# Optimization experiments

Measured on AMD Instinct MI355X. Metric: run time of the kernel, lower is better.

The kernel has to match this reference:

```python
import jax, jax.numpy as jnp
import numpy as np

S, B, D, H, L = 1024, 2, 1024, 16, 4
HD = D // H            # 64
MLP = 4 * D            # 4096
EPS = 1e-5


def _ln(x, w, b):
    m = x.mean(-1, keepdims=True)
    v = ((x - m) ** 2).mean(-1, keepdims=True)
    return (x - m) * jax.lax.rsqrt(v + EPS) * w + b


def _rotate_half(x):
    h = x.shape[-1] // 2
    return jnp.concatenate([-x[..., h:], x[..., :h]], axis=-1)


def _rope(t, cos, sin):
    # t: (B, S, H, HD); cos/sin: (S, HD) broadcast to (1, S, 1, HD)
    return t * cos[None, :, None, :] + _rotate_half(t) * sin[None, :, None, :]


def setup_inputs() -> dict:
    key = jax.random.key(0)
    ks = iter(jax.random.split(key, 64))

    def p(shape, scale=0.02):
        return jax.random.normal(next(ks), shape, jnp.float32) * scale

    return {
        "x": jax.random.normal(next(ks), (S, B, D), jnp.float32),
        "rotary_pos_emb": jax.random.normal(next(ks), (S, HD // 2), jnp.float32),
        # stacked per-layer params (leading dim L) for lax.scan
        "ln1_w": jnp.ones((L, D), jnp.float32), "ln1_b": jnp.zeros((L, D), jnp.float32),
        "in_w": p((L, 3 * D, D)), "in_b": jnp.zeros((L, 3 * D), jnp.float32),
        "out_w": p((L, D, D)), "out_b": jnp.zeros((L, D), jnp.float32),
        "ln2_w": jnp.ones((L, D), jnp.float32), "ln2_b": jnp.zeros((L, D), jnp.float32),
        "fc_w": p((L, MLP, D)), "fc_b": jnp.zeros((L, MLP), jnp.float32),
        "cp_w": p((L, D, MLP)), "cp_b": jnp.zeros((L, D), jnp.float32),
        # attention pooling head (qkv_bias=False in CrossAttention)
        "pn_q_w": jnp.ones((D,), jnp.float32), "pn_q_b": jnp.zeros((D,), jnp.float32),
        "pn_k_w": jnp.ones((D,), jnp.float32), "pn_k_b": jnp.zeros((D,), jnp.float32),
        "pn_v_w": jnp.ones((D,), jnp.float32), "pn_v_b": jnp.zeros((D,), jnp.float32),
        "pq_w": p((D, D)), "pk_w": p((D, D)), "pv_w": p((D, D)),
        "pp_w": p((D, D)), "pp_b": jnp.zeros((D,), jnp.float32),
    }


def reference(x, rotary_pos_emb, ln1_w, ln1_b, in_w, in_b, out_w, out_b,
              ln2_w, ln2_b, fc_w, fc_b, cp_w, cp_b,
              pn_q_w, pn_q_b, pn_k_w, pn_k_b, pn_v_w, pn_v_b,
              pq_w, pk_w, pv_w, pp_w, pp_b):
    # freqs (S, HD/2) -> cos/sin tiled twice along last dim: (S, HD)
    cos = jnp.tile(jnp.cos(rotary_pos_emb), (1, 2))
    sin = jnp.tile(jnp.sin(rotary_pos_emb), (1, 2))
    scale = 1.0 / np.sqrt(HD).astype(np.float32)

    def layer(h, p):
        l1w, l1b, iw, ib, ow, ob, l2w, l2b, fw, fb, cw, cb = p
        a = _ln(h, l1w, l1b)
        qkv = jnp.einsum('sbd,ed->sbe', a, iw) + ib           # (S,B,3D)
        qkv = qkv.reshape(S, B, 3, H, HD)
        q = jnp.transpose(qkv[:, :, 0], (1, 0, 2, 3))          # (B,S,H,HD)
        k = jnp.transpose(qkv[:, :, 1], (1, 0, 2, 3))
        v = jnp.transpose(qkv[:, :, 2], (1, 0, 2, 3))
        q = _rope(q, cos, sin)
        k = _rope(k, cos, sin)
        q, k, v = (t.transpose(0, 2, 1, 3) for t in (q, k, v))  # (B,H,S,HD)
        attn = jax.nn.softmax(jnp.einsum('bhsd,bhtd->bhst', q, k) * scale, axis=-1)
        o = jnp.einsum('bhst,bhtd->bhsd', attn, v)
        o = o.transpose(2, 0, 1, 3).reshape(S, B, D)           # back to (S,B,D)
        h = h + jnp.einsum('sbd,ed->sbe', o, ow) + ob          # residual + out_proj
        m = _ln(h, l2w, l2b)
        m = jax.nn.gelu(jnp.einsum('sbd,ed->sbe', m, fw) + fb, approximate=False)
        h = h + jnp.einsum('sbe,de->sbd', m, cw) + cb          # residual + c_proj
        return h, None

    h, _ = jax.lax.scan(layer, x, (ln1_w, ln1_b, in_w, in_b, out_w, out_b,
                                   ln2_w, ln2_b, fc_w, fc_b, cp_w, cp_b))

    # AttentionPoolingBlock: mean-pooled single query, cross-attend over tokens
    t = h.transpose(1, 0, 2)                                   # (B,N,C)
    xq = _ln(t.mean(1, keepdims=True), pn_q_w, pn_q_b)         # (B,1,C)
    xk = _ln(t, pn_k_w, pn_k_b)
    xv = _ln(t, pn_v_w, pn_v_b)
    q = (xq @ pq_w.T).reshape(B, 1, H, HD).transpose(0, 2, 1, 3)   # (B,H,1,HD)
    k = (xk @ pk_w.T).reshape(B, S, H, HD).transpose(0, 2, 1, 3)
    v = (xv @ pv_w.T).reshape(B, S, H, HD).transpose(0, 2, 1, 3)
    a = jax.nn.softmax(jnp.einsum('bhqd,bhtd->bhqt', q, k) * scale, axis=-1)
    o = jnp.einsum('bhqt,bhtd->bhqd', a, v).transpose(0, 2, 1, 3).reshape(B, 1, D)
    return (o @ pp_w.T + pp_b)[:, 0]                           # (B, D)
```

## Files before the change

### kernel.cpp

```cpp
#include <hip/hip_runtime.h>
#include <math.h>

#define S_LEN  1024
#define BATCH  2
#define DMODEL 1024
#define NHEAD  16
#define HDIM   64
#define NLAYER 4
#define MLPD   4096
#define MROWS  (S_LEN*BATCH)

typedef __attribute__((ext_vector_type(8))) short bf16x8_t;
typedef __attribute__((ext_vector_type(4))) float f32x4_t;

__device__ __forceinline__ unsigned short f2bf(float f) {
  union { float f; unsigned u; } c; c.f = f;
  return (unsigned short)((c.u + 0x7FFFu + ((c.u >> 16) & 1u)) >> 16);
}
__device__ __forceinline__ float bf2f(unsigned short u) {
  union { unsigned u; float f; } c; c.u = ((unsigned)u) << 16; return c.f;
}

__device__ __forceinline__ void gl_lds16(const unsigned short* g, unsigned short* l) {
  __builtin_amdgcn_global_load_lds(
      (const __attribute__((address_space(1))) unsigned int*)(g),
      (__attribute__((address_space(3))) unsigned int*)(l), 16, 0, 0);
}

template<int CTRL>
__device__ __forceinline__ float dpp16(float x) {
  return __int_as_float(__builtin_amdgcn_update_dpp(
      0, __float_as_int(x), CTRL, 0xf, 0xf, true));
}
__device__ __forceinline__ float rowmax16(float x) {
  x = fmaxf(x, dpp16<0x128>(x));
  x = fmaxf(x, dpp16<0x124>(x));
  x = fmaxf(x, dpp16<0x122>(x));
  x = fmaxf(x, dpp16<0x121>(x));
  return x;
}
__device__ __forceinline__ float rowsum16(float x) {
  x += dpp16<0x128>(x);
  x += dpp16<0x124>(x);
  x += dpp16<0x122>(x);
  x += dpp16<0x121>(x);
  return x;
}

__global__ __launch_bounds__(256) void w2bf_kernel(const float* __restrict__ src,
    unsigned short* __restrict__ dst, int n) {
  const int i = (blockIdx.x * 256 + threadIdx.x) * 8;
  if (i >= n) return;
  float4 v0 = *(const float4*)(src + i);
  float4 v1 = *(const float4*)(src + i + 4);
  ushort4 u0, u1;
  u0.x = f2bf(v0.x); u0.y = f2bf(v0.y); u0.z = f2bf(v0.z); u0.w = f2bf(v0.w);
  u1.x = f2bf(v1.x); u1.y = f2bf(v1.y); u1.z = f2bf(v1.z); u1.w = f2bf(v1.w);
  *(ushort4*)(dst + i)     = u0;
  *(ushort4*)(dst + i + 4) = u1;
}

__global__ __launch_bounds__(256) void trig_kernel(const float* __restrict__ rot,
    float2* __restrict__ tab) {
  const int i = blockIdx.x * 256 + threadIdx.x;
  const float f = rot[i];
  tab[i] = make_float2(cosf(f), sinf(f));
}

template<bool BF16OUT>
__global__ __launch_bounds__(256) void ln_kernel(const float* __restrict__ x,
    const float* __restrict__ w, const float* __restrict__ b,
    void* __restrict__ out, float inscale) {
  const int row = blockIdx.x;
  const int tid = threadIdx.x;
  const float* xr = x + (size_t)row * DMODEL;
  float4 v = *(const float4*)(xr + tid * 4);
  v.x *= inscale; v.y *= inscale; v.z *= inscale; v.w *= inscale;
  float s1 = v.x + v.y + v.z + v.w;
  float s2 = v.x*v.x + v.y*v.y + v.z*v.z + v.w*v.w;
  #pragma unroll
  for (int off = 32; off; off >>= 1) {
    s1 += __shfl_xor(s1, off);
    s2 += __shfl_xor(s2, off);
  }
  __shared__ float as1[4], as2[4];
  if ((tid & 63) == 0) { as1[tid >> 6] = s1; as2[tid >> 6] = s2; }
  __syncthreads();
  s1 = as1[0] + as1[1] + as1[2] + as1[3];
  s2 = as2[0] + as2[1] + as2[2] + as2[3];
  const float mean = s1 * (1.0f / DMODEL);
  const float var  = s2 * (1.0f / DMODEL) - mean * mean;
  const float r = rsqrtf(var + 1e-5f);
  float4 wv = *(const float4*)(w + tid * 4);
  float4 bv = *(const float4*)(b + tid * 4);
  float o0 = (v.x - mean) * r * wv.x + bv.x;
  float o1 = (v.y - mean) * r * wv.y + bv.y;
  float o2 = (v.z - mean) * r * wv.z + bv.z;
  float o3 = (v.w - mean) * r * wv.w + bv.w;
  if (BF16OUT) {
    ushort4 u; u.x = f2bf(o0); u.y = f2bf(o1); u.z = f2bf(o2); u.w = f2bf(o3);
    *(ushort4*)((unsigned short*)out + (size_t)row * DMODEL + tid * 4) = u;
  } else {
    float4 ov; ov.x = o0; ov.y = o1; ov.z = o2; ov.w = o3;
    *(float4*)((float*)out + (size_t)row * DMODEL + tid * 4) = ov;
  }
}

template<int NS, bool ADDDEST, bool DOLN>
__global__ __launch_bounds__(256) void reduce_ln_kernel(
    const float* __restrict__ part, const float* __restrict__ bias,
    float* __restrict__ dest, const float* __restrict__ lnw,
    const float* __restrict__ lnb, unsigned short* __restrict__ lnout) {
  const int row = blockIdx.x;
  const int tid = threadIdx.x;
  const size_t off = (size_t)row * DMODEL + tid * 4;
  float4 v;
  if (ADDDEST) v = *(const float4*)(dest + off);
  else { v.x = 0.f; v.y = 0.f; v.z = 0.f; v.w = 0.f; }
  if (bias) {
    float4 b4 = *(const float4*)(bias + tid * 4);
    v.x += b4.x; v.y += b4.y; v.z += b4.z; v.w += b4.w;
  }
  #pragma unroll
  for (int z = 0; z < NS; ++z) {
    float4 p = *(const float4*)(part + (size_t)z * (MROWS * DMODEL) + off);
    v.x += p.x; v.y += p.y; v.z += p.z; v.w += p.w;
  }
  *(float4*)(dest + off) = v;
  if (DOLN) {
    float s1 = v.x + v.y + v.z + v.w;
    float s2 = v.x*v.x + v.y*v.y + v.z*v.z + v.w*v.w;
    #pragma unroll
    for (int o = 32; o; o >>= 1) {
      s1 += __shfl_xor(s1, o);
      s2 += __shfl_xor(s2, o);
    }
    __shared__ float as1[4], as2[4];
    if ((tid & 63) == 0) { as1[tid >> 6] = s1; as2[tid >> 6] = s2; }
    __syncthreads();
    s1 = as1[0] + as1[1] + as1[2] + as1[3];
    s2 = as2[0] + as2[1] + as2[2] + as2[3];
    const float mean = s1 * (1.0f / DMODEL);
    const float var  = s2 * (1.0f / DMODEL) - mean * mean;
    const float r = rsqrtf(var + 1e-5f);
    float4 wv = *(const float4*)(lnw + tid * 4);
    float4 bv = *(const float4*)(lnb + tid * 4);
    ushort4 u;
    u.x = f2bf((v.x - mean) * r * wv.x + bv.x);
    u.y = f2bf((v.y - mean) * r * wv.y + bv.y);
    u.z = f2bf((v.z - mean) * r * wv.z + bv.z);
    u.w = f2bf((v.w - mean) * r * wv.w + bv.w);
    *(ushort4*)(lnout + (size_t)row * DMODEL + tid * 4) = u;
  }
}

template<int SPLIT, bool GELU, bool PARTIAL, bool OUTBF16, bool ROPE>
__global__ __launch_bounds__(256, 3) void gemm_mfma(
    const unsigned short* __restrict__ A, const unsigned short* __restrict__ W,
    const float* __restrict__ bias, void* __restrict__ Cout,
    int M, int N, int K,
    const float2* __restrict__ trig, unsigned short* __restrict__ qt,
    unsigned short* __restrict__ kt) {
  constexpr int BK = 32;
  __shared__ __align__(16) unsigned short As[3][128 * BK];
  __shared__ __align__(16) unsigned short Bs[3][128 * BK];
  const int tid  = threadIdx.x;
  const int wid  = tid >> 6;
  const int lane = tid & 63;
  const int lrow = lane & 15;
  const int lq   = lane >> 4;

  const int NB = gridDim.x, MB = gridDim.y;
  const int f = blockIdx.y * NB + blockIdx.x;
  const int xcd = f & 7;
  const int idx = f >> 3;
  const int m0 = (idx % MB) * 128;
  const int n0 = (xcd + (idx / MB) * 8) * 128;

  const int wm = (wid >> 1) * 64;
  const int wn = (wid & 1) * 64;
  const int Kc = K / SPLIT;
  const int kbase = blockIdx.z * Kc;
  const int nt = Kc / BK;

  f32x4_t acc[4][4];
  #pragma unroll
  for (int i = 0; i < 4; ++i)
    #pragma unroll
    for (int j = 0; j < 4; ++j) acc[i][j] = (f32x4_t){0.f, 0.f, 0.f, 0.f};

  const int c1 = tid, c2 = tid + 256;
  const int r1c = c1 >> 2, r2c = c2 >> 2;
  const int kc1 = ((c1 & 3) ^ ((r1c >> 1) & 3)) * 8;
  const int kc2 = ((c2 & 3) ^ ((r2c >> 1) & 3)) * 8;
  const unsigned short* Ag1 = A + (size_t)(m0 + r1c) * K + kbase + kc1;
  const unsigned short* Ag2 = A + (size_t)(m0 + r2c) * K + kbase + kc2;
  const unsigned short* Wg1 = W + (size_t)(n0 + r1c) * K + kbase + kc1;
  const unsigned short* Wg2 = W + (size_t)(n0 + r2c) * K + kbase + kc2;
  const int l1 = c1 * 8, l2 = c2 * 8;

  auto stage = [&](int t, int b) {
    const int ko = t * BK;
    gl_lds16(Ag1 + ko, &As[b][l1]);
    gl_lds16(Ag2 + ko, &As[b][l2]);
    gl_lds16(Wg1 + ko, &Bs[b][l1]);
    gl_lds16(Wg2 + ko, &Bs[b][l2]);
  };
  auto compute = [&](int b) {
    bf16x8_t af[4], bfr[4];
    #pragma unroll
    for (int i = 0; i < 4; ++i) {
      const int row = wm + i * 16 + lrow;
      const int ch  = lq ^ ((row >> 1) & 3);
      af[i] = *(const bf16x8_t*)&As[b][row * BK + ch * 8];
    }
    #pragma unroll
    for (int j = 0; j < 4; ++j) {
      const int row = wn + j * 16 + lrow;
      const int ch  = lq ^ ((row >> 1) & 3);
      bfr[j] = *(const bf16x8_t*)&Bs[b][row * BK + ch * 8];
    }
    #pragma unroll
    for (int i = 0; i < 4; ++i)
      #pragma unroll
      for (int j = 0; j < 4; ++j)
        acc[i][j] = __builtin_amdgcn_mfma_f32_16x16x32_bf16(af[i], bfr[j], acc[i][j], 0, 0, 0);
  };

  stage(0, 0);
  stage(1, 1);

  int cr = 0;
  int cs = 2;
  for (int t = 0; t < nt - 1; ++t) {
    asm volatile("s_waitcnt vmcnt(4)" ::: "memory");
    __builtin_amdgcn_sched_barrier(0);
    __builtin_amdgcn_s_barrier();
    __builtin_amdgcn_sched_barrier(0);
    if (t + 2 < nt) stage(t + 2, cs);
    compute(cr);
    cr = (cr == 2) ? 0 : cr + 1;
    cs = (cs == 2) ? 0 : cs + 1;
  }
  asm volatile("s_waitcnt vmcnt(0)" ::: "memory");
  __builtin_amdgcn_sched_barrier(0);
  __builtin_amdgcn_s_barrier();
  __builtin_amdgcn_sched_barrier(0);
  compute(cr);

  float bj[4];
  #pragma unroll
  for (int j = 0; j < 4; ++j)
    bj[j] = (bias && (SPLIT == 1 || blockIdx.z == 0)) ? bias[n0 + wn + j * 16 + lrow] : 0.f;

  if (ROPE) {
    const int strip = n0 + wn;
    const int which = strip >> 10;
    const int head  = (strip >> 6) & 15;
    #pragma unroll
    for (int i = 0; i < 4; ++i) {
      #pragma unroll
      for (int r = 0; r < 4; ++r) {
        const int row = m0 + wm + i * 16 + lq * 4 + r;
        const int s = row >> 1, b = row & 1;
        if (which == 2) {
          const size_t idx2 = (size_t)row * N + strip + lrow;
          #pragma unroll
          for (int j = 0; j < 4; ++j)
            ((unsigned short*)Cout)[idx2 + j * 16] = f2bf(acc[i][j][r] + bj[j]);
        } else {
          unsigned short* dst = (which == 0 ? qt : kt)
              + (((size_t)(b * 16 + head) * 1024 + s) << 6);
          #pragma unroll
          for (int j = 0; j < 4; ++j) {
            const int d = j * 16 + lrow;
            const float2 tt = trig[s * 32 + (d & 31)];
            const float sign = (j < 2) ? -1.0f : 1.0f;
            const float val = acc[i][j][r] + bj[j];
            const float par = acc[i][j ^ 2][r] + bj[j ^ 2];
            dst[d] = f2bf(val * tt.x + sign * par * tt.y);
          }
        }
      }
    }
  } else {
    const size_t zoff = PARTIAL ? (size_t)blockIdx.z * ((size_t)M * N) : 0;
    #pragma unroll
    for (int i = 0; i < 4; ++i) {
      #pragma unroll
      for (int r = 0; r < 4; ++r) {
        const int row = m0 + wm + i * 16 + lq * 4 + r;
        const size_t idx2 = (size_t)row * N + n0 + wn + lrow;
        #pragma unroll
        for (int j = 0; j < 4; ++j) {
          float val = acc[i][j][r] + bj[j];
          if (GELU)
            val = 0.5f * val * (1.0f + erff(val * 0.70710678118654752f));
          if (PARTIAL)
            ((float*)Cout)[zoff + idx2 + j * 16] = val;
          else if (OUTBF16)
            ((unsigned short*)Cout)[idx2 + j * 16] = f2bf(val);
          else
            ((float*)Cout)[idx2 + j * 16] = val;
        }
      }
    }
  }
}

__global__ __launch_bounds__(256) void vtrans_kernel(const unsigned short* __restrict__ qkv,
    unsigned short* __restrict__ vt) {
  const int bh = blockIdx.x >> 4;
  const int s0 = (blockIdx.x & 15) * 64;
  const int b = bh >> 4, hh = bh & 15;
  __shared__ unsigned short Vl[64 * 72];
  const int t = threadIdx.x;
  const int sl = t >> 2, dcol = (t & 3) * 16;
  const unsigned short* src = qkv + (size_t)((s0 + sl) * 2 + b) * 3072 + 2048 + hh * 64 + dcol;
  uint4 a = *(const uint4*)(src);
  uint4 c = *(const uint4*)(src + 8);
  *(uint4*)&Vl[sl * 72 + dcol]     = a;
  *(uint4*)&Vl[sl * 72 + dcol + 8] = c;
  __syncthreads();
  const int dr = t >> 2, soff = (t & 3) * 16;
  unsigned short o[16];
  #pragma unroll
  for (int i = 0; i < 16; ++i) o[i] = Vl[(soff + i) * 72 + dr];
  unsigned short* dst = vt + (((size_t)bh * 64 + dr) << 10) + s0 + soff;
  *(uint4*)(dst)     = *(uint4*)(o);
  *(uint4*)(dst + 8) = *(uint4*)(o + 8);
}

__global__ __launch_bounds__(256, 3) void attn_kernel(
    const unsigned short* __restrict__ q, const unsigned short* __restrict__ k,
    const unsigned short* __restrict__ vtr, unsigned short* __restrict__ o) {
  const int tid  = threadIdx.x;
  const int wid  = tid >> 6;
  const int lane = tid & 63;
  const int col  = lane & 15;
  const int quad = lane >> 4;
  const int bh   = blockIdx.x >> 4;
  const int qw   = (blockIdx.x & 15) * 64 + wid * 16;

  __shared__ __align__(16) unsigned short Ks[64 * 72];
  __shared__ __align__(16) unsigned short Vs[64 * 72];
  __shared__ __align__(16) unsigned short Pl_[4][16 * 72];
  unsigned short* Pl = Pl_[wid];

  const unsigned short* kb = k   + ((size_t)bh << 16);
  const unsigned short* vb = vtr + ((size_t)bh << 16);

  bf16x8_t qa0, qa1;
  {
    const unsigned short* qp = q + ((((size_t)bh << 10) + qw + col) << 6) + quad * 8;
    qa0 = *(const bf16x8_t*)(qp);
    qa1 = *(const bf16x8_t*)(qp + 32);
  }

  f32x4_t oacc[4];
  #pragma unroll
  for (int j = 0; j < 4; ++j) oacc[j] = (f32x4_t){0.f, 0.f, 0.f, 0.f};
  float mr[4] = {-3.0e38f, -3.0e38f, -3.0e38f, -3.0e38f};
  float lr[4] = {0.f, 0.f, 0.f, 0.f};

  const int srow = tid >> 2;
  const int scol = (tid & 3) * 16;
  const unsigned short* gk0 = kb + (size_t)srow * 64 + scol;
  const unsigned short* gv0 = vb + (size_t)srow * 1024 + scol;
  unsigned short* lk0 = &Ks[srow * 72 + scol];
  unsigned short* lv0 = &Vs[srow * 72 + scol];

  {
    uint4 ka = *(const uint4*)(gk0);
    uint4 kc = *(const uint4*)(gk0 + 8);
    uint4 va = *(const uint4*)(gv0);
    uint4 vc = *(const uint4*)(gv0 + 8);
    *(uint4*)(lk0)     = ka;
    *(uint4*)(lk0 + 8) = kc;
    *(uint4*)(lv0)     = va;
    *(uint4*)(lv0 + 8) = vc;
  }
  __syncthreads();

  for (int t0 = 0; t0 < 1024; t0 += 64) {
    const bool more = (t0 + 64) < 1024;
    uint4 nka, nkc, nva, nvc;
    if (more) {
      const unsigned short* gk = gk0 + (size_t)(t0 + 64) * 64;
      const unsigned short* gv = gv0 + (t0 + 64);
      nka = *(const uint4*)(gk);
      nkc = *(const uint4*)(gk + 8);
      nva = *(const uint4*)(gv);
      nvc = *(const uint4*)(gv + 8);
    }

    f32x4_t sc[4];
    #pragma unroll
    for (int j = 0; j < 4; ++j) {
      bf16x8_t kf0 = *(const bf16x8_t*)&Ks[(j * 16 + col) * 72 + quad * 8];
      bf16x8_t kf1 = *(const bf16x8_t*)&Ks[(j * 16 + col) * 72 + quad * 8 + 32];
      f32x4_t c = (f32x4_t){0.f, 0.f, 0.f, 0.f};
      c = __builtin_amdgcn_mfma_f32_16x16x32_bf16(qa0, kf0, c, 0, 0, 0);
      c = __builtin_amdgcn_mfma_f32_16x16x32_bf16(qa1, kf1, c, 0, 0, 0);
      sc[j] = c;
    }

    #pragma unroll
    for (int r = 0; r < 4; ++r) {
      float s0 = sc[0][r] * 0.125f, s1 = sc[1][r] * 0.125f;
      float s2 = sc[2][r] * 0.125f, s3 = sc[3][r] * 0.125f;
      const float rm = rowmax16(fmaxf(fmaxf(s0, s1), fmaxf(s2, s3)));
      if (__any(rm > mr[r])) {
        const float mn = fmaxf(mr[r], rm);
        const float alpha = __expf(mr[r] - mn);
        mr[r] = mn;
        lr[r] *= alpha;
        #pragma unroll
        for (int j = 0; j < 4; ++j) oacc[j][r] *= alpha;
      }
      const float m = mr[r];
      const float p0 = __expf(s0 - m), p1 = __expf(s1 - m);
      const float p2 = __expf(s2 - m), p3 = __expf(s3 - m);
      lr[r] += rowsum16(p0 + p1 + p2 + p3);
      const int prow = (quad * 4 + r) * 72;
      Pl[prow +  0 + col] = f2bf(p0);
      Pl[prow + 16 + col] = f2bf(p1);
      Pl[prow + 32 + col] = f2bf(p2);
      Pl[prow + 48 + col] = f2bf(p3);
    }

    bf16x8_t pa0 = *(const bf16x8_t*)&Pl[col * 72 + quad * 8];
    bf16x8_t pa1 = *(const bf16x8_t*)&Pl[col * 72 + quad * 8 + 32];
    #pragma unroll
    for (int j = 0; j < 4; ++j) {
      bf16x8_t vf0 = *(const bf16x8_t*)&Vs[(j * 16 + col) * 72 + quad * 8];
      bf16x8_t vf1 = *(const bf16x8_t*)&Vs[(j * 16 + col) * 72 + quad * 8 + 32];
      oacc[j] = __builtin_amdgcn_mfma_f32_16x16x32_bf16(pa0, vf0, oacc[j], 0, 0, 0);
      oacc[j] = __builtin_amdgcn_mfma_f32_16x16x32_bf16(pa1, vf1, oacc[j], 0, 0, 0);
    }

    __syncthreads();
    if (more) {
      *(uint4*)(lk0)     = nka;
      *(uint4*)(lk0 + 8) = nkc;
      *(uint4*)(lv0)     = nva;
      *(uint4*)(lv0 + 8) = nvc;
    }
    __syncthreads();
  }

  const int b = bh >> 4, hh = bh & 15;
  #pragma unroll
  for (int r = 0; r < 4; ++r) {
    const float inv = 1.0f / lr[r];
    const int sq = qw + quad * 4 + r;
    unsigned short* orow = o + (((size_t)sq * 2 + b) << 10) + hh * 64;
    #pragma unroll
    for (int j = 0; j < 4; ++j)
      orow[j * 16 + col] = f2bf(oacc[j][r] * inv);
  }
}

__global__ __launch_bounds__(256) void mean_kernel(const float* __restrict__ h,
    float* __restrict__ tsum) {
  const int idx = blockIdx.x * 256 + threadIdx.x;
  const int bd = idx & 2047;
  const int sc = idx >> 11;
  const int b = bd >> 10, d = bd & 1023;
  float sm = 0.f;
  for (int s = sc * 128; s < sc * 128 + 128; ++s)
    sm += h[(((size_t)s * 2 + b) << 10) + d];
  atomicAdd(&tsum[bd], sm);
}

__global__ __launch_bounds__(256) void smallmv_kernel(const float* __restrict__ in,
    const float* __restrict__ W, const float* __restrict__ bias,
    float* __restrict__ out) {
  const int lane = threadIdx.x & 63;
  const int n = blockIdx.x * 4 + (threadIdx.x >> 6);
  const int b = blockIdx.y;
  const float* wr = W + (size_t)n * 1024;
  const float* xr = in + (size_t)b * 1024;
  float sm = 0.f;
  #pragma unroll
  for (int j = 0; j < 4; ++j) {
    float4 wv = *(const float4*)(wr + lane * 4 + j * 256);
    float4 xv = *(const float4*)(xr + lane * 4 + j * 256);
    sm += wv.x * xv.x + wv.y * xv.y + wv.z * xv.z + wv.w * xv.w;
  }
  #pragma unroll
  for (int off = 32; off; off >>= 1) sm += __shfl_xor(sm, off);
  if (lane == 0) out[(size_t)b * 1024 + n] = sm + (bias ? bias[n] : 0.f);
}

__global__ __launch_bounds__(256) void pool_attn_part(const float* __restrict__ q,
    const float* __restrict__ k, const float* __restrict__ v,
    float* __restrict__ part) {
  const int wid  = (blockIdx.x * 256 + threadIdx.x) >> 6;
  const int lane = threadIdx.x & 63;
  const int bh = wid >> 4, kblk = wid & 15;
  const int b = bh >> 4, hh = bh & 15;
  const float qd = q[(size_t)b * 1024 + hh * 64 + lane];
  float mx = -3.0e38f, l = 0.f, acc = 0.f;
  for (int t = kblk * 64; t < kblk * 64 + 64; ++t) {
    const size_t ro = (((size_t)t * 2 + b) << 10) + hh * 64 + lane;
    float p = qd * k[ro];
    p += __shfl_xor(p, 32); p += __shfl_xor(p, 16); p += __shfl_xor(p, 8);
    p += __shfl_xor(p, 4);  p += __shfl_xor(p, 2);  p += __shfl_xor(p, 1);
    const float sc = p * 0.125f;
    const float mn = fmaxf(mx, sc);
    const float alpha = __expf(mx - mn);
    const float w = __expf(sc - mn);
    acc = acc * alpha + w * v[ro];
    l   = l * alpha + w;
    mx  = mn;
  }
  float* pp = part + (size_t)wid * 68;
  if (lane == 0) { pp[0] = mx; pp[1] = l; }
  pp[4 + lane] = acc;
}

__global__ __launch_bounds__(256) void pool_attn_comb(const float* __restrict__ part,
    float* __restrict__ o) {
  const int wid  = (blockIdx.x * 256 + threadIdx.x) >> 6;
  const int lane = threadIdx.x & 63;
  const float* pb = part + (size_t)wid * 16 * 68;
  float M = -3.0e38f;
  #pragma unroll
  for (int w = 0; w < 16; ++w) M = fmaxf(M, pb[w * 68]);
  float L = 0.f, O = 0.f;
  #pragma unroll
  for (int w = 0; w < 16; ++w) {
    const float e = __expf(pb[w * 68] - M);
    L += e * pb[w * 68 + 1];
    O += e * pb[w * 68 + 4 + lane];
  }
  const int b = wid >> 4, hh = wid & 15;
  o[(size_t)b * 1024 + hh * 64 + lane] = O / L;
}

extern "C" void kernel_launch(void* const* d_in, const int* in_sizes, int n_in,
                              void* d_out, int out_size, void* d_ws, size_t ws_size,
                              hipStream_t stream) {
  (void)in_sizes; (void)n_in; (void)out_size; (void)ws_size;
  const float* x     = (const float*)d_in[0];
  const float* rot   = (const float*)d_in[1];
  const float* ln1_w = (const float*)d_in[2];
  const float* ln1_b = (const float*)d_in[3];
  const float* in_w  = (const float*)d_in[4];
  const float* in_b  = (const float*)d_in[5];
  const float* out_w = (const float*)d_in[6];
  const float* out_b = (const float*)d_in[7];
  const float* ln2_w = (const float*)d_in[8];
  const float* ln2_b = (const float*)d_in[9];
  const float* fc_w  = (const float*)d_in[10];
  const float* fc_b  = (const float*)d_in[11];
  const float* cp_w  = (const float*)d_in[12];
  const float* cp_b  = (const float*)d_in[13];
  const float* pn_q_w = (const float*)d_in[14];
  const float* pn_q_b = (const float*)d_in[15];
  const float* pn_k_w = (const float*)d_in[16];
  const float* pn_k_b = (const float*)d_in[17];
  const float* pn_v_w = (const float*)d_in[18];
  const float* pn_v_b = (const float*)d_in[19];
  const float* pq_w  = (const float*)d_in[20];
  const float* pk_w  = (const float*)d_in[21];
  const float* pv_w  = (const float*)d_in[22];
  const float* pp_w  = (const float*)d_in[23];
  const float* pp_b  = (const float*)d_in[24];

  float* ws = (float*)d_ws;
  const size_t M1 = 1u << 20;
  float* h  = ws;
  float* a  = ws + 2 * M1;
  float* r1 = ws + 4 * M1;
  float* qt = ws + 12 * M1;
  float* kt = ws + 14 * M1;
  float* vt = ws + 16 * M1;
  float* o  = ws + 18 * M1;
  float* trig = ws + 19 * M1;
  float* wbf = ws + 20 * M1;
  unsigned short* a_bf  = (unsigned short*)a;
  unsigned short* r1_bf = (unsigned short*)r1;
  unsigned short* o_bf  = (unsigned short*)o;
  unsigned short* qt_bf = (unsigned short*)qt;
  unsigned short* kt_bf = (unsigned short*)kt;
  unsigned short* vt_bf = (unsigned short*)vt;
  unsigned short* wb_qkv_all = (unsigned short*)wbf;
  unsigned short* wb_out_all = wb_qkv_all + 12582912;
  unsigned short* wb_fc_all  = wb_out_all + 4194304;
  unsigned short* wb_cp_all  = wb_fc_all  + 16777216;
  float* part_op = r1;
  float* part_cp = qt;
  float* part_pool = ws + 5 * M1;
  float* tsum  = qt;
  float* xq    = qt + 2048;
  float* qpool = qt + 4096;
  float* opool = qt + 6144;
  float* ppart = qt + 8192;

  hipMemcpyAsync(h, x, 2 * M1 * sizeof(float), hipMemcpyDeviceToDevice, stream);

  trig_kernel<<<128, 256, 0, stream>>>(rot, (float2*)trig);
  ln_kernel<true><<<MROWS, 256, 0, stream>>>(h, ln1_w, ln1_b, a_bf, 1.0f);
  w2bf_kernel<<<12582912 / 2048, 256, 0, stream>>>(in_w,  wb_qkv_all, 12582912);
  w2bf_kernel<<<4194304  / 2048, 256, 0, stream>>>(out_w, wb_out_all, 4194304);
  w2bf_kernel<<<16777216 / 2048, 256, 0, stream>>>(fc_w,  wb_fc_all,  16777216);
  w2bf_kernel<<<16777216 / 2048, 256, 0, stream>>>(cp_w,  wb_cp_all,  16777216);

  for (int l = 0; l < NLAYER; ++l) {
    const unsigned short* wb_qkv = wb_qkv_all + (size_t)l * 3145728;
    const unsigned short* wb_out = wb_out_all + (size_t)l * 1048576;
    const unsigned short* wb_fc  = wb_fc_all  + (size_t)l * 4194304;
    const unsigned short* wb_cp  = wb_cp_all  + (size_t)l * 4194304;

    gemm_mfma<1, false, false, true, true><<<dim3(3072 / 128, MROWS / 128, 1), 256, 0, stream>>>(
        a_bf, wb_qkv, in_b + l * 3072, r1_bf, MROWS, 3072, 1024,
        (const float2*)trig, qt_bf, kt_bf);
    vtrans_kernel<<<512, 256, 0, stream>>>(r1_bf, vt_bf);
    attn_kernel<<<512, 256, 0, stream>>>(qt_bf, kt_bf, vt_bf, o_bf);
    gemm_mfma<4, false, true, false, false><<<dim3(1024 / 128, MROWS / 128, 4), 256, 0, stream>>>(
        o_bf, wb_out, nullptr, part_op, MROWS, 1024, 1024, nullptr, nullptr, nullptr);
    reduce_ln_kernel<4, true, true><<<MROWS, 256, 0, stream>>>(
        part_op, out_b + l * 1024, h, ln2_w + l * DMODEL, ln2_b + l * DMODEL, a_bf);
    gemm_mfma<1, true, false, true, false><<<dim3(4096 / 128, MROWS / 128, 1), 256, 0, stream>>>(
        a_bf, wb_fc, fc_b + l * 4096, r1_bf, MROWS, 4096, 1024, nullptr, nullptr, nullptr);
    gemm_mfma<4, false, true, false, false><<<dim3(1024 / 128, MROWS / 128, 4), 256, 0, stream>>>(
        r1_bf, wb_cp, nullptr, part_cp, MROWS, 1024, 4096, nullptr, nullptr, nullptr);
    if (l < NLAYER - 1)
      reduce_ln_kernel<4, true, true><<<MROWS, 256, 0, stream>>>(
          part_cp, cp_b + l * 1024, h,
          ln1_w + (l + 1) * DMODEL, ln1_b + (l + 1) * DMODEL, a_bf);
    else
      reduce_ln_kernel<4, true, false><<<MROWS, 256, 0, stream>>>(
          part_cp, cp_b + l * 1024, h, nullptr, nullptr, nullptr);
  }

  hipMemsetAsync(tsum, 0, 2048 * sizeof(float), stream);
  mean_kernel<<<64, 256, 0, stream>>>(h, tsum);
  ln_kernel<false><<<BATCH, 256, 0, stream>>>(tsum, pn_q_w, pn_q_b, xq, 1.0f / S_LEN);
  ln_kernel<true><<<MROWS, 256, 0, stream>>>(h, pn_k_w, pn_k_b, a_bf, 1.0f);
  ln_kernel<true><<<MROWS, 256, 0, stream>>>(h, pn_v_w, pn_v_b, r1_bf, 1.0f);
  smallmv_kernel<<<dim3(256, BATCH), 256, 0, stream>>>(xq, pq_w, nullptr, qpool);
  unsigned short* wb_pk = wb_qkv_all;
  unsigned short* wb_pv = wb_qkv_all + 1048576;
  w2bf_kernel<<<1048576 / 2048, 256, 0, stream>>>(pk_w, wb_pk, 1048576);
  w2bf_kernel<<<1048576 / 2048, 256, 0, stream>>>(pv_w, wb_pv, 1048576);
  gemm_mfma<2, false, true, false, false><<<dim3(1024 / 128, MROWS / 128, 2), 256, 0, stream>>>(
      a_bf, wb_pk, nullptr, part_pool, MROWS, 1024, 1024, nullptr, nullptr, nullptr);
  reduce_ln_kernel<2, false, false><<<MROWS, 256, 0, stream>>>(
      part_pool, nullptr, kt, nullptr, nullptr, nullptr);
  gemm_mfma<2, false, true, false, false><<<dim3(1024 / 128, MROWS / 128, 2), 256, 0, stream>>>(
      r1_bf, wb_pv, nullptr, part_pool, MROWS, 1024, 1024, nullptr, nullptr, nullptr);
  reduce_ln_kernel<2, false, false><<<MROWS, 256, 0, stream>>>(
      part_pool, nullptr, vt, nullptr, nullptr, nullptr);
  pool_attn_part<<<128, 256, 0, stream>>>(qpool, kt, vt, ppart);
  pool_attn_comb<<<8, 256, 0, stream>>>(ppart, opool);
  smallmv_kernel<<<dim3(256, BATCH), 256, 0, stream>>>(opool, pp_w, pp_b, (float*)d_out);
}
```

Before: 1.048 ms.

## Split attention blocks to two waves covering 32 queries each

The attention kernel now launches 1024 blocks of 128 threads, each handling 32 query rows with two wavefronts, instead of 512 blocks of 256 threads handling 64 rows. The K/V tile staging is redistributed so each thread copies 32 elements per row instead of 16. This spreads the 512 attention work items across more blocks to fill the 256 CUs more evenly. The cost is that each K/V tile is loaded from global memory twice as often overall, and each thread holds more prefetch registers.

```diff
diff --git a/kernel.cpp b/kernel.cpp
--- a/kernel.cpp
+++ b/kernel.cpp
@@ -331,7 +331,7 @@
   *(uint4*)(dst + 8) = *(uint4*)(o + 8);
 }
 
-__global__ __launch_bounds__(256, 3) void attn_kernel(
+__global__ __launch_bounds__(128, 2) void attn_kernel(
     const unsigned short* __restrict__ q, const unsigned short* __restrict__ k,
     const unsigned short* __restrict__ vtr, unsigned short* __restrict__ o) {
   const int tid  = threadIdx.x;
@@ -339,12 +339,12 @@
   const int lane = tid & 63;
   const int col  = lane & 15;
   const int quad = lane >> 4;
-  const int bh   = blockIdx.x >> 4;
-  const int qw   = (blockIdx.x & 15) * 64 + wid * 16;
+  const int bh   = blockIdx.x >> 5;
+  const int qw   = (blockIdx.x & 31) * 32 + wid * 16;
 
   __shared__ __align__(16) unsigned short Ks[64 * 72];
   __shared__ __align__(16) unsigned short Vs[64 * 72];
-  __shared__ __align__(16) unsigned short Pl_[4][16 * 72];
+  __shared__ __align__(16) unsigned short Pl_[2][16 * 72];
   unsigned short* Pl = Pl_[wid];
 
   const unsigned short* kb = k   + ((size_t)bh << 16);
@@ -363,35 +363,33 @@
   float mr[4] = {-3.0e38f, -3.0e38f, -3.0e38f, -3.0e38f};
   float lr[4] = {0.f, 0.f, 0.f, 0.f};
 
-  const int srow = tid >> 2;
-  const int scol = (tid & 3) * 16;
+  const int srow = tid >> 1;
+  const int scol = (tid & 1) * 32;
   const unsigned short* gk0 = kb + (size_t)srow * 64 + scol;
   const unsigned short* gv0 = vb + (size_t)srow * 1024 + scol;
   unsigned short* lk0 = &Ks[srow * 72 + scol];
   unsigned short* lv0 = &Vs[srow * 72 + scol];
 
   {
-    uint4 ka = *(const uint4*)(gk0);
-    uint4 kc = *(const uint4*)(gk0 + 8);
-    uint4 va = *(const uint4*)(gv0);
-    uint4 vc = *(const uint4*)(gv0 + 8);
-    *(uint4*)(lk0)     = ka;
-    *(uint4*)(lk0 + 8) = kc;
-    *(uint4*)(lv0)     = va;
-    *(uint4*)(lv0 + 8) = vc;
+    #pragma unroll
+    for (int c = 0; c < 4; ++c) {
+      *(uint4*)(lk0 + c * 8) = *(const uint4*)(gk0 + c * 8);
+      *(uint4*)(lv0 + c * 8) = *(const uint4*)(gv0 + c * 8);
+    }
   }
   __syncthreads();
 
   for (int t0 = 0; t0 < 1024; t0 += 64) {
     const bool more = (t0 + 64) < 1024;
-    uint4 nka, nkc, nva, nvc;
+    uint4 nk[4], nv[4];
     if (more) {
       const unsigned short* gk = gk0 + (size_t)(t0 + 64) * 64;
       const unsigned short* gv = gv0 + (t0 + 64);
-      nka = *(const uint4*)(gk);
-      nkc = *(const uint4*)(gk + 8);
-      nva = *(const uint4*)(gv);
-      nvc = *(const uint4*)(gv + 8);
+      #pragma unroll
+      for (int c = 0; c < 4; ++c) {
+        nk[c] = *(const uint4*)(gk + c * 8);
+        nv[c] = *(const uint4*)(gv + c * 8);
+      }
     }
 
     f32x4_t sc[4];
@@ -441,10 +439,11 @@
 
     __syncthreads();
     if (more) {
-      *(uint4*)(lk0)     = nka;
-      *(uint4*)(lk0 + 8) = nkc;
-      *(uint4*)(lv0)     = nva;
-      *(uint4*)(lv0 + 8) = nvc;
+      #pragma unroll
+      for (int c = 0; c < 4; ++c) {
+        *(uint4*)(lk0 + c * 8) = nk[c];
+        *(uint4*)(lv0 + c * 8) = nv[c];
+      }
     }
     __syncthreads();
   }
@@ -618,7 +617,7 @@
         a_bf, wb_qkv, in_b + l * 3072, r1_bf, MROWS, 3072, 1024,
         (const float2*)trig, qt_bf, kt_bf);
     vtrans_kernel<<<512, 256, 0, stream>>>(r1_bf, vt_bf);
-    attn_kernel<<<512, 256, 0, stream>>>(qt_bf, kt_bf, vt_bf, o_bf);
+    attn_kernel<<<1024, 128, 0, stream>>>(qt_bf, kt_bf, vt_bf, o_bf);
     gemm_mfma<4, false, true, false, false><<<dim3(1024 / 128, MROWS / 128, 4), 256, 0, stream>>>(
         o_bf, wb_out, nullptr, part_op, MROWS, 1024, 1024, nullptr, nullptr, nullptr);
     reduce_ln_kernel<4, true, true><<<MROWS, 256, 0, stream>>>(
```

New measurement: 1.238 ms. +18.1%, slower.

## Split attention key range across two half-blocks and merge partial softmax

Applied to the files above, without the earlier changes.

Doubles the attention block to 512 threads, with each half processing half of the key/value sequence using its own LDS buffers. Partial outputs, running max and sum from the second half are written to shared memory and combined with the first half's using log-sum-exp rescaling. This aims to raise parallelism and halve the serial key loop per wave, at the cost of more LDS per block and an extra merge step.

```diff
diff --git a/kernel.cpp b/kernel.cpp
--- a/kernel.cpp
+++ b/kernel.cpp
@@ -331,20 +331,23 @@
   *(uint4*)(dst + 8) = *(uint4*)(o + 8);
 }
 
-__global__ __launch_bounds__(256, 3) void attn_kernel(
+__global__ __launch_bounds__(512, 4) void attn_kernel(
     const unsigned short* __restrict__ q, const unsigned short* __restrict__ k,
     const unsigned short* __restrict__ vtr, unsigned short* __restrict__ o) {
   const int tid  = threadIdx.x;
   const int wid  = tid >> 6;
+  const int qg   = wid & 3;
+  const int half = tid >> 8;
   const int lane = tid & 63;
   const int col  = lane & 15;
   const int quad = lane >> 4;
   const int bh   = blockIdx.x >> 4;
-  const int qw   = (blockIdx.x & 15) * 64 + wid * 16;
-
-  __shared__ __align__(16) unsigned short Ks[64 * 72];
-  __shared__ __align__(16) unsigned short Vs[64 * 72];
-  __shared__ __align__(16) unsigned short Pl_[4][16 * 72];
+  const int qw   = (blockIdx.x & 15) * 64 + qg * 16;
+  const int tbase = half * 512;
+
+  __shared__ __align__(16) unsigned short Ks[2][64 * 72];
+  __shared__ __align__(16) unsigned short Vs[2][64 * 72];
+  __shared__ __align__(16) unsigned short Pl_[8][16 * 72];
   unsigned short* Pl = Pl_[wid];
 
   const unsigned short* kb = k   + ((size_t)bh << 16);
@@ -363,12 +366,13 @@
   float mr[4] = {-3.0e38f, -3.0e38f, -3.0e38f, -3.0e38f};
   float lr[4] = {0.f, 0.f, 0.f, 0.f};
 
-  const int srow = tid >> 2;
-  const int scol = (tid & 3) * 16;
-  const unsigned short* gk0 = kb + (size_t)srow * 64 + scol;
-  const unsigned short* gv0 = vb + (size_t)srow * 1024 + scol;
-  unsigned short* lk0 = &Ks[srow * 72 + scol];
-  unsigned short* lv0 = &Vs[srow * 72 + scol];
+  const int ht   = tid & 255;
+  const int srow = ht >> 2;
+  const int scol = (ht & 3) * 16;
+  const unsigned short* gk0 = kb + (size_t)(tbase + srow) * 64 + scol;
+  const unsigned short* gv0 = vb + (size_t)srow * 1024 + tbase + scol;
+  unsigned short* lk0 = &Ks[half][srow * 72 + scol];
+  unsigned short* lv0 = &Vs[half][srow * 72 + scol];
 
   {
     uint4 ka = *(const uint4*)(gk0);
@@ -382,8 +386,8 @@
   }
   __syncthreads();
 
-  for (int t0 = 0; t0 < 1024; t0 += 64) {
-    const bool more = (t0 + 64) < 1024;
+  for (int t0 = 0; t0 < 512; t0 += 64) {
+    const bool more = (t0 + 64) < 512;
     uint4 nka, nkc, nva, nvc;
     if (more) {
       const unsigned short* gk = gk0 + (size_t)(t0 + 64) * 64;
@@ -397,8 +401,8 @@
     f32x4_t sc[4];
     #pragma unroll
     for (int j = 0; j < 4; ++j) {
-      bf16x8_t kf0 = *(const bf16x8_t*)&Ks[(j * 16 + col) * 72 + quad * 8];
-      bf16x8_t kf1 = *(const bf16x8_t*)&Ks[(j * 16 + col) * 72 + quad * 8 + 32];
+      bf16x8_t kf0 = *(const bf16x8_t*)&Ks[half][(j * 16 + col) * 72 + quad * 8];
+      bf16x8_t kf1 = *(const bf16x8_t*)&Ks[half][(j * 16 + col) * 72 + quad * 8 + 32];
       f32x4_t c = (f32x4_t){0.f, 0.f, 0.f, 0.f};
       c = __builtin_amdgcn_mfma_f32_16x16x32_bf16(qa0, kf0, c, 0, 0, 0);
       c = __builtin_amdgcn_mfma_f32_16x16x32_bf16(qa1, kf1, c, 0, 0, 0);
@@ -433,8 +437,8 @@
     bf16x8_t pa1 = *(const bf16x8_t*)&Pl[col * 72 + quad * 8 + 32];
     #pragma unroll
     for (int j = 0; j < 4; ++j) {
-      bf16x8_t vf0 = *(const bf16x8_t*)&Vs[(j * 16 + col) * 72 + quad * 8];
-      bf16x8_t vf1 = *(const bf16x8_t*)&Vs[(j * 16 + col) * 72 + quad * 8 + 32];
+      bf16x8_t vf0 = *(const bf16x8_t*)&Vs[half][(j * 16 + col) * 72 + quad * 8];
+      bf16x8_t vf1 = *(const bf16x8_t*)&Vs[half][(j * 16 + col) * 72 + quad * 8 + 32];
       oacc[j] = __builtin_amdgcn_mfma_f32_16x16x32_bf16(pa0, vf0, oacc[j], 0, 0, 0);
       oacc[j] = __builtin_amdgcn_mfma_f32_16x16x32_bf16(pa1, vf1, oacc[j], 0, 0, 0);
     }
@@ -449,15 +453,35 @@
     __syncthreads();
   }
 
-  const int b = bh >> 4, hh = bh & 15;
-  #pragma unroll
-  for (int r = 0; r < 4; ++r) {
-    const float inv = 1.0f / lr[r];
-    const int sq = qw + quad * 4 + r;
-    unsigned short* orow = o + (((size_t)sq * 2 + b) << 10) + hh * 64;
-    #pragma unroll
-    for (int j = 0; j < 4; ++j)
-      orow[j * 16 + col] = f2bf(oacc[j][r] * inv);
+  float* sm = (float*)Ks;
+  __syncthreads();
+  if (half == 1) {
+    #pragma unroll
+    for (int r = 0; r < 4; ++r) {
+      const int ro = quad * 4 + r;
+      float* row = sm + (size_t)(qg * 16 + ro) * 68;
+      #pragma unroll
+      for (int j = 0; j < 4; ++j) row[j * 16 + col] = oacc[j][r];
+      if (col == 0) { row[64] = mr[r]; row[65] = lr[r]; }
+    }
+  }
+  __syncthreads();
+  if (half == 0) {
+    const int b = bh >> 4, hh = bh & 15;
+    #pragma unroll
+    for (int r = 0; r < 4; ++r) {
+      const int ro = quad * 4 + r;
+      const float* row = sm + (size_t)(qg * 16 + ro) * 68;
+      const float m1 = row[64], l1 = row[65];
+      const float M = fmaxf(mr[r], m1);
+      const float e0 = __expf(mr[r] - M), e1 = __expf(m1 - M);
+      const float inv = 1.0f / (e0 * lr[r] + e1 * l1);
+      const int sq = qw + ro;
+      unsigned short* orow = o + (((size_t)sq * 2 + b) << 10) + hh * 64;
+      #pragma unroll
+      for (int j = 0; j < 4; ++j)
+        orow[j * 16 + col] = f2bf((oacc[j][r] * e0 + row[j * 16 + col] * e1) * inv);
+    }
   }
 }
 
@@ -618,7 +642,7 @@
         a_bf, wb_qkv, in_b + l * 3072, r1_bf, MROWS, 3072, 1024,
         (const float2*)trig, qt_bf, kt_bf);
     vtrans_kernel<<<512, 256, 0, stream>>>(r1_bf, vt_bf);
-    attn_kernel<<<512, 256, 0, stream>>>(qt_bf, kt_bf, vt_bf, o_bf);
+    attn_kernel<<<512, 512, 0, stream>>>(qt_bf, kt_bf, vt_bf, o_bf);
     gemm_mfma<4, false, true, false, false><<<dim3(1024 / 128, MROWS / 128, 4), 256, 0, stream>>>(
         o_bf, wb_out, nullptr, part_op, MROWS, 1024, 1024, nullptr, nullptr, nullptr);
     reduce_ln_kernel<4, true, true><<<MROWS, 256, 0, stream>>>(
```

After: 1.026 ms. 1.02x faster.
